# Optimization experiments

Measured on AMD Instinct MI355X. Metric: run time of the kernel, lower is better.

Reference implementation:

```python
import jax, jax.numpy as jnp
import numpy as np
from jax import lax

B, T, N, D = 64, 128, 64, 64
Q, EMB, PLM = 5, 8, 768
ALPHA = 0.5  # rarity_alpha

def _mlp(x, W1, b1, W2, b2):
    return jax.nn.relu(x @ W1 + b1) @ W2 + b2

def setup_inputs() -> dict:
    key = jax.random.key(0)
    ks = jax.random.split(key, 16)
    def xav(k, shape):
        fan_in = shape[-2] if len(shape) > 1 else shape[0]
        return jax.random.normal(k, shape, jnp.float32) / np.sqrt(fan_in)
    obs_emb = jax.random.normal(ks[0], (B, T, N, D), jnp.float32)
    observed_mask = (jax.random.uniform(ks[1], (B, T, N)) < 0.5).astype(jnp.float32)
    lengths = jax.random.randint(ks[2], (B, 1), T // 2, T + 1).astype(jnp.int32)
    lengths = lengths.at[0, 0].set(T)  # ensure max(lengths) == T like torch loop bound
    avg_interval = jax.random.uniform(ks[3], (B, T, N), jnp.float32) * 10.0
    return {
        "obs_emb": obs_emb, "observed_mask": observed_mask,
        "lengths": lengths, "avg_interval": avg_interval,
        "var_plm_rep": jax.random.normal(ks[4], (N, PLM), jnp.float32),
        "rarity_W": jax.random.normal(ks[5], (N, N), jnp.float32),
        "Wf1": xav(ks[6], (PLM, 2 * D)), "bf1": jnp.zeros((2 * D,), jnp.float32),
        "Wf2": xav(ks[7], (2 * D, Q)), "bf2": jnp.zeros((Q,), jnp.float32),
        "Wg1": xav(ks[8], (PLM, 2 * D)), "bg1": jnp.zeros((2 * D,), jnp.float32),
        "Wg2": xav(ks[9], (2 * D, EMB)), "bg2": jnp.zeros((EMB,), jnp.float32),
        "Wu": xav(ks[10], (Q, 2 * D + 1, D)), "bu": xav(ks[11], (Q, D)),
        "Wr": xav(ks[12], (Q, 2 * D + 1, D)), "br": xav(ks[13], (Q, D)),
        "Wc": xav(ks[14], (Q, 2 * D + 1, D)), "bc": xav(ks[15], (Q, D)),
    }

def reference(obs_emb, observed_mask, lengths, avg_interval, var_plm_rep, rarity_W,
              Wf1, bf1, Wf2, bf2, Wg1, bg1, Wg2, bg2, Wu, bu, Wr, br, Wc, bc):
    Bb, Tt, Nn, Dd = obs_emb.shape
    m_all = observed_mask.astype(obs_emb.dtype)                 # [B,T,N]
    # plm reps are repeated across batch in torch -> batch-identical, keep [N,*]
    qv = _mlp(var_plm_rep, Wf1, bf1, Wf2, bf2)                  # [N,Q]
    ne = _mlp(var_plm_rep, Wg1, bg1, Wg2, bg2)                  # [N,EMB]
    ne = ne / jnp.linalg.norm(ne, axis=-1, keepdims=True)
    adj = jax.nn.softmax(ne @ ne.T, axis=-1)                    # [N,N]
    # time-invariant per-node hypernetwork weights (MLP_Param einsums hoisted)
    Wr_n = jnp.einsum('nq,qio->nio', qv, Wr); br_n = qv @ br    # [N,2D+1,D],[N,D]
    Wu_n = jnp.einsum('nq,qio->nio', qv, Wu); bu_n = qv @ bu
    Wc_n = jnp.einsum('nq,qio->nio', qv, Wc); bc_n = qv @ bc
    I = jnp.eye(Nn, dtype=obs_emb.dtype)
    var_total = m_all.sum(axis=1)                               # [B,N]
    lens = lengths[:, 0]

    def step(carry, inp):
        h, out = carry
        x_t, m_t, ai_t, t = inp                                 # [B,N,D],[B,N],[B,N],[]
        rs = ALPHA * jnp.tanh(ai_t / (var_total + 1.0))         # rarity score [B,N]
        x = jnp.concatenate([x_t, rs[..., None]], axis=-1)      # [B,N,D+1]
        combined = jnp.concatenate([x, h], axis=-1)             # [B,N,2D+1]
        R = -rarity_W[None] * jnp.abs(rs[:, :, None] - rs[:, None, :])
        am = m_t[:, :, None] * m_t[:, None, :]                  # masked adjacency support
        A = adj[None] * (1.0 + R) * am * (1.0 - I) + I          # [B,N,N]
        msg = jnp.einsum('bij,bjf->bif', A, combined)           # dense message passing
        r = jax.nn.sigmoid(jnp.einsum('bnf,nfo->bno', msg, Wr_n) + br_n)
        u = jax.nn.sigmoid(jnp.einsum('bnf,nfo->bno', msg, Wu_n) + bu_n)
        upd = m_t[..., None] > 0                                # observed-node scatter mask
        h_r = jnp.where(upd, r * h, h)
        comb2 = jnp.concatenate([x, h_r], axis=-1)              # NOTE: no adj matmul here (as in torch)
        cand = jnp.tanh(jnp.einsum('bnf,nfo->bno', comb2, Wc_n) + bc_n)
        h_new = jnp.where(upd, (1.0 - u) * h_r + u * cand, h)
        out_new = jnp.where((t == lens - 1)[:, None, None], h_new, out)
        return (h_new, out_new), None

    h0 = jnp.zeros((Bb, Nn, Dd), obs_emb.dtype)
    xs = (obs_emb.swapaxes(0, 1), m_all.swapaxes(0, 1),
          avg_interval.swapaxes(0, 1), jnp.arange(Tt))
    (_, out), _ = lax.scan(step, (h0, jnp.zeros_like(h0)), xs)
    return out
```

## Files before the change

### kernel.cpp

```cpp
#include <hip/hip_runtime.h>
#include <cstddef>
#include <cstdint>

#define B_ 64
#define T_ 128
#define N_ 64
#define D_ 64
#define Q_ 5
#define E_ 8
#define P_ 768
#define H_ 128

typedef _Float16 f16;
typedef _Float16 f16x2 __attribute__((ext_vector_type(2)));
typedef _Float16 f16x4 __attribute__((ext_vector_type(4)));
typedef _Float16 f16x8 __attribute__((ext_vector_type(8)));
typedef float f32x4 __attribute__((ext_vector_type(4)));

__device__ __forceinline__ float fast_sig(float x) {
  return 1.f / (1.f + __expf(-x));
}
__device__ __forceinline__ float fast_tanh(float x) {
  return 1.f - 2.f / (1.f + __expf(2.f * x));
}
__device__ __forceinline__ f16x8 splat8(f16 c) {
  return f16x8{c, c, c, c, c, c, c, c};
}

__global__ void k_mlps(const float* __restrict__ vpr,
                       const float* __restrict__ Wf1, const float* __restrict__ bf1,
                       const float* __restrict__ Wf2, const float* __restrict__ bf2,
                       const float* __restrict__ Wg1, const float* __restrict__ bg1,
                       const float* __restrict__ Wg2, const float* __restrict__ bg2,
                       float* __restrict__ qv, float* __restrict__ neb) {
  int n = blockIdx.x;
  int tid = threadIdx.x;
  __shared__ float v[P_];
  __shared__ float hf[H_];
  __shared__ float hg[H_];
  __shared__ float tmp[E_];

  for (int i = tid; i < P_; i += 256) v[i] = vpr[n * P_ + i];
  __syncthreads();

  if (tid < H_) {
    int j = tid;
    float a = bf1[j];
#pragma unroll 8
    for (int i = 0; i < P_; ++i) a += v[i] * Wf1[i * H_ + j];
    hf[j] = fmaxf(a, 0.f);
  } else {
    int j = tid - H_;
    float a = bg1[j];
#pragma unroll 8
    for (int i = 0; i < P_; ++i) a += v[i] * Wg1[i * H_ + j];
    hg[j] = fmaxf(a, 0.f);
  }
  __syncthreads();
  if (tid < Q_) {
    float a = bf2[tid];
    for (int j = 0; j < H_; ++j) a += hf[j] * Wf2[j * Q_ + tid];
    qv[n * Q_ + tid] = a;
  } else if (tid >= 8 && tid < 8 + E_) {
    int e = tid - 8;
    float a = bg2[e];
    for (int j = 0; j < H_; ++j) a += hg[j] * Wg2[j * E_ + e];
    tmp[e] = a;
  }
  __syncthreads();
  if (tid == 0) {
    float s = 0.f;
    for (int e = 0; e < E_; ++e) s += tmp[e] * tmp[e];
    float r = 1.f / sqrtf(s);
    for (int e = 0; e < E_; ++e) neb[n * E_ + e] = tmp[e] * r;
  }
}

__global__ void k_meta(const float* __restrict__ neb, const float* __restrict__ qv,
                       const float* __restrict__ br, const float* __restrict__ bu,
                       const float* __restrict__ bc,
                       const float* __restrict__ Wr, const float* __restrict__ Wu,
                       const float* __restrict__ Wc, const float* __restrict__ rarw,
                       f16x2* __restrict__ adjP, float* __restrict__ brn,
                       float* __restrict__ bun, float* __restrict__ bcn,
                       float* __restrict__ WrsR, float* __restrict__ WrsU,
                       float* __restrict__ WrsC) {
  int n = blockIdx.x;
  int j = threadIdx.x;
  float s = 0.f;
#pragma unroll
  for (int e = 0; e < E_; ++e) s += neb[n * E_ + e] * neb[j * E_ + e];
  float m = s;
  for (int off = 32; off; off >>= 1) m = fmaxf(m, __shfl_xor(m, off));
  float ex = __expf(s - m);
  float sum = ex;
  for (int off = 32; off; off >>= 1) sum += __shfl_xor(sum, off);
  float av = ex / sum;
  adjP[n * N_ + j] = f16x2{(f16)av, (f16)(av * rarw[n * N_ + j])};

  float pr = 0.f, pu = 0.f, pc = 0.f;
  float wr = 0.f, wu = 0.f, wc = 0.f;
#pragma unroll
  for (int q = 0; q < Q_; ++q) {
    float qq = qv[n * Q_ + q];
    pr += qq * br[q * D_ + j];
    pu += qq * bu[q * D_ + j];
    pc += qq * bc[q * D_ + j];
    wr += qq * Wr[((size_t)q * 129 + 64) * D_ + j];
    wu += qq * Wu[((size_t)q * 129 + 64) * D_ + j];
    wc += qq * Wc[((size_t)q * 129 + 64) * D_ + j];
  }
  brn[n * D_ + j] = pr;
  bun[n * D_ + j] = pu;
  bcn[n * D_ + j] = pc;
  WrsR[n * D_ + j] = wr;
  WrsU[n * D_ + j] = wu;
  WrsC[n * D_ + j] = wc;
}

__global__ void k_pack(const float* __restrict__ Wr, const float* __restrict__ Wu,
                       const float* __restrict__ Wc, f16* __restrict__ Wpk) {
  int bid = blockIdx.x;
  int nt = bid & 3;
  int kt = (bid >> 2) & 3;
  int q = (bid >> 4) % 5;
  int g = bid / 80;
  const float* W = (g == 0) ? Wr : ((g == 1) ? Wu : Wc);
  int l = threadIdx.x;
  int co = 16 * nt + (l & 15);
  f16* dst = Wpk + (size_t)bid * 512 + l * 8;
#pragma unroll
  for (int e = 0; e < 8; ++e) {
    int k = 32 * kt + 8 * (l >> 4) + e;
    int f = k + (k >= 64);
    dst[e] = (f16)W[((size_t)q * 129 + f) * D_ + co];
  }
}

__global__ void k_vt(const float* __restrict__ mask, float* __restrict__ vt) {
  int b = blockIdx.x;
  int n = threadIdx.x;
  float s = 0.f;
  for (int t = 0; t < T_; ++t) s += mask[(b * T_ + t) * N_ + n];
  vt[b * N_ + n] = s;
}

__global__ __launch_bounds__(256, 1) __attribute__((amdgpu_waves_per_eu(1, 1)))
void k_seq(const float* __restrict__ obs, const float* __restrict__ mask,
           const int* __restrict__ lengths, const float* __restrict__ ai,
           const f16x2* __restrict__ adjP,
           const float* __restrict__ brn, const float* __restrict__ bun,
           const float* __restrict__ bcn, const float* __restrict__ WrsR,
           const float* __restrict__ WrsU, const float* __restrict__ WrsC,
           const float* __restrict__ qv, const float* __restrict__ vt,
           const f16* __restrict__ Wpk, float* __restrict__ out) {
  __shared__ __align__(16) f16 combT[128 * 72];
  __shared__ __align__(16) f16 xA[64 * 72];
  __shared__ __align__(16) f16 actA[64 * 168];
  __shared__ __align__(16) f16 AP[64 * 88];
  __shared__ __align__(16) f16 qvS[64 * 8];
  __shared__ __align__(16) float rsS[N_];
  __shared__ __align__(16) float mS[N_];
  __shared__ __align__(16) float mrS[N_];

  const int tid = threadIdx.x;
  const int b = blockIdx.x;
  const int lane = tid & 63;
  const int wv = tid >> 6;
  const int lm = lane & 15;
  const int lq = lane >> 4;
  const int oc = 16 * wv + lm;

  const int pn = tid >> 2;
  const int pj = 16 * (tid & 3);

  f16x8 wW[3][4][5];
#pragma unroll
  for (int g = 0; g < 3; ++g)
#pragma unroll
    for (int kt = 0; kt < 4; ++kt)
#pragma unroll
      for (int q = 0; q < 5; ++q)
        wW[g][kt][q] = *(const f16x8*)(Wpk +
            ((size_t)(((g * 5 + q) * 4 + kt) * 4 + wv) * 64 + lane) * 8);

  f16x2 bR[8], bU[8], bC[8], wRs[8], wUs[8], wCs[8];
#pragma unroll
  for (int mt = 0; mt < 4; ++mt)
#pragma unroll
    for (int ii = 0; ii < 2; ++ii) {
      int n0 = 16 * mt + 4 * lq + 2 * ii;
      bR[2 * mt + ii]  = f16x2{(f16)brn[n0 * D_ + oc],  (f16)brn[(n0 + 1) * D_ + oc]};
      bU[2 * mt + ii]  = f16x2{(f16)bun[n0 * D_ + oc],  (f16)bun[(n0 + 1) * D_ + oc]};
      bC[2 * mt + ii]  = f16x2{(f16)bcn[n0 * D_ + oc],  (f16)bcn[(n0 + 1) * D_ + oc]};
      wRs[2 * mt + ii] = f16x2{(f16)WrsR[n0 * D_ + oc], (f16)WrsR[(n0 + 1) * D_ + oc]};
      wUs[2 * mt + ii] = f16x2{(f16)WrsU[n0 * D_ + oc], (f16)WrsU[(n0 + 1) * D_ + oc]};
      wCs[2 * mt + ii] = f16x2{(f16)WrsC[n0 * D_ + oc], (f16)WrsC[(n0 + 1) * D_ + oc]};
    }

  f16x2 adjR[16];
#pragma unroll
  for (int k = 0; k < 16; ++k) adjR[k] = adjP[pn * N_ + pj + k];

#pragma unroll
  for (int u2 = 0; u2 < 2; ++u2) {
    int idx = 2 * tid + u2;
    int n = idx >> 3, q = idx & 7;
    qvS[idx] = (q < Q_) ? (f16)qv[n * Q_ + q] : (f16)0.f;
  }
  for (int i = tid; i < 64 * 72; i += 256) combT[64 * 72 + i] = (f16)0.f;

  f32x4 h[4];
#pragma unroll
  for (int mt = 0; mt < 4; ++mt) h[mt] = f32x4{0.f, 0.f, 0.f, 0.f};

  const float* xb = obs + (size_t)b * T_ * (N_ * D_) + pn * D_ + pj;
  float4 xq0 = *(const float4*)(xb);
  float4 xq1 = *(const float4*)(xb + 4);
  float4 xq2 = *(const float4*)(xb + 8);
  float4 xq3 = *(const float4*)(xb + 12);
  float mCur = 0.f, aCur = 0.f, vtR = 0.f;
  if (tid < N_) {
    vtR = vt[b * N_ + tid];
    mCur = mask[(size_t)b * T_ * N_ + tid];
    aCur = ai[(size_t)b * T_ * N_ + tid];
  }
  const int lenm1 = lengths[b] - 1;
  __syncthreads();

  f16x8 qh[4];
#pragma unroll
  for (int mt = 0; mt < 4; ++mt) qh[mt] = *(const f16x8*)(qvS + (lm + 16 * mt) * 8);

  for (int t = 0; t < T_; ++t) {
    if (tid < N_) {
      mS[tid] = mCur;
      rsS[tid] = 0.5f * fast_tanh(aCur / (vtR + 1.f));
    }
    {
      f16x8 v0 = {(f16)xq0.x, (f16)xq0.y, (f16)xq0.z, (f16)xq0.w,
                  (f16)xq1.x, (f16)xq1.y, (f16)xq1.z, (f16)xq1.w};
      f16x8 v1 = {(f16)xq2.x, (f16)xq2.y, (f16)xq2.z, (f16)xq2.w,
                  (f16)xq3.x, (f16)xq3.y, (f16)xq3.z, (f16)xq3.w};
      *(f16x8*)(xA + pn * 72 + pj) = v0;
      *(f16x8*)(xA + pn * 72 + pj + 8) = v1;
    }
    __syncthreads();

    {
      float ri = rsS[pn], mi = mS[pn];
      f16x8 av0, av1;
#pragma unroll
      for (int k = 0; k < 16; ++k) {
        float a = ((float)adjR[k][0] -
                   (float)adjR[k][1] * fabsf(ri - rsS[pj + k])) * mi * mS[pj + k];
        if (pn == pj + k) a = 1.f;
        if (k < 8) av0[k] = (f16)a;
        else av1[k - 8] = (f16)a;
      }
      *(f16x8*)(AP + pn * 88 + pj) = av0;
      *(f16x8*)(AP + pn * 88 + pj + 8) = av1;

      int n0 = 16 * wv;
      f16x8 t0, t1;
#pragma unroll
      for (int k = 0; k < 8; ++k) t0[k] = xA[(n0 + k) * 72 + lane];
#pragma unroll
      for (int k = 0; k < 8; ++k) t1[k] = xA[(n0 + 8 + k) * 72 + lane];
      *(f16x8*)(combT + lane * 72 + n0) = t0;
      *(f16x8*)(combT + lane * 72 + n0 + 8) = t1;
    }
    __syncthreads();

    {
#pragma unroll
      for (int s = 0; s < 2; ++s) {
        int ft = 2 * wv + s;
#pragma unroll
        for (int mt = 0; mt < 4; ++mt) {
          f32x4 acc = {0.f, 0.f, 0.f, 0.f};
#pragma unroll
          for (int kt = 0; kt < 2; ++kt) {
            f16x8 aF = *(const f16x8*)(AP + (lm + 16 * mt) * 88 + 8 * lq + 32 * kt);
            f16x8 bF = *(const f16x8*)(combT + (lm + 16 * ft) * 72 + 8 * lq + 32 * kt);
            acc = __builtin_amdgcn_mfma_f32_16x16x32_f16(aF, bF, acc, 0, 0, 0);
          }
          int row = 16 * mt + 4 * lq;
          int col = 16 * ft + lm;
          actA[(row + 0) * 168 + col] = (f16)acc[0];
          actA[(row + 1) * 168 + col] = (f16)acc[1];
          actA[(row + 2) * 168 + col] = (f16)acc[2];
          actA[(row + 3) * 168 + col] = (f16)acc[3];
        }
      }
      f16x8 a0 = *(const f16x8*)(AP + pn * 88 + pj);
      f16x8 a1 = *(const f16x8*)(AP + pn * 88 + pj + 8);
      float s = 0.f;
#pragma unroll
      for (int k = 0; k < 8; ++k)
        s += (float)a0[k] * rsS[pj + k] + (float)a1[k] * rsS[pj + 8 + k];
      s += __shfl_xor(s, 1);
      s += __shfl_xor(s, 2);
      if ((tid & 3) == 0) mrS[pn] = s;
    }
    __syncthreads();

    f32x4 racc[4], uacc[4];
#pragma unroll
    for (int mt = 0; mt < 4; ++mt) {
      racc[mt] = f32x4{0.f, 0.f, 0.f, 0.f};
      uacc[mt] = f32x4{0.f, 0.f, 0.f, 0.f};
    }
#pragma unroll
    for (int kt = 0; kt < 4; ++kt) {
      f16x8 aF[4];
#pragma unroll
      for (int mt = 0; mt < 4; ++mt)
        aF[mt] = *(const f16x8*)(actA + (lm + 16 * mt) * 168 + 8 * lq + 32 * kt);
#pragma unroll
      for (int q = 0; q < 5; ++q) {
#pragma unroll
        for (int mt = 0; mt < 4; ++mt) {
          f16x8 as = aF[mt] * splat8(qh[mt][q]);
          racc[mt] = __builtin_amdgcn_mfma_f32_16x16x32_f16(as, wW[0][kt][q], racc[mt], 0, 0, 0);
          uacc[mt] = __builtin_amdgcn_mfma_f32_16x16x32_f16(as, wW[1][kt][q], uacc[mt], 0, 0, 0);
        }
      }
    }

    f16x2 upk[8], hrpk[8];
    {
#pragma unroll
      for (int mt = 0; mt < 4; ++mt) {
        float4 mr4 = *(const float4*)&mrS[16 * mt + 4 * lq];
        float4 m4 = *(const float4*)&mS[16 * mt + 4 * lq];
#pragma unroll
        for (int i = 0; i < 4; ++i) {
          int row = 16 * mt + 4 * lq + i;
          int ii = 2 * mt + (i >> 1);
          float pr = racc[mt][i] + (float)bR[ii][i & 1] + mr4[i] * (float)wRs[ii][i & 1];
          float pu = uacc[mt][i] + (float)bU[ii][i & 1] + mr4[i] * (float)wUs[ii][i & 1];
          float r = fast_sig(pr);
          float u = fast_sig(pu);
          float hr = (m4[i] > 0.f) ? r * h[mt][i] : h[mt][i];
          upk[ii][i & 1] = (f16)u;
          hrpk[ii][i & 1] = (f16)hr;
          AP[row * 88 + oc] = (f16)hr;
        }
      }
      if (t + 1 < T_) {
        const float* xn = xb + (size_t)(t + 1) * (N_ * D_);
        xq0 = *(const float4*)(xn);
        xq1 = *(const float4*)(xn + 4);
        xq2 = *(const float4*)(xn + 8);
        xq3 = *(const float4*)(xn + 12);
        if (tid < N_) {
          mCur = mask[((size_t)b * T_ + t + 1) * N_ + tid];
          aCur = ai[((size_t)b * T_ + t + 1) * N_ + tid];
        }
      }
    }
    __syncthreads();

    f32x4 cacc[4];
#pragma unroll
    for (int mt = 0; mt < 4; ++mt) cacc[mt] = f32x4{0.f, 0.f, 0.f, 0.f};
#pragma unroll
    for (int kt = 0; kt < 4; ++kt) {
      f16x8 aF[4];
#pragma unroll
      for (int mt = 0; mt < 4; ++mt) {
        if (kt < 2)
          aF[mt] = *(const f16x8*)(xA + (lm + 16 * mt) * 72 + 8 * lq + 32 * kt);
        else
          aF[mt] = *(const f16x8*)(AP + (lm + 16 * mt) * 88 + 8 * lq + 32 * (kt - 2));
      }
#pragma unroll
      for (int q = 0; q < 5; ++q) {
#pragma unroll
        for (int mt = 0; mt < 4; ++mt) {
          f16x8 as = aF[mt] * splat8(qh[mt][q]);
          cacc[mt] = __builtin_amdgcn_mfma_f32_16x16x32_f16(as, wW[2][kt][q], cacc[mt], 0, 0, 0);
        }
      }
    }

    {
#pragma unroll
      for (int mt = 0; mt < 4; ++mt) {
        float4 rs4 = *(const float4*)&rsS[16 * mt + 4 * lq];
        float4 m4 = *(const float4*)&mS[16 * mt + 4 * lq];
        f16x4 hq;
#pragma unroll
        for (int i = 0; i < 4; ++i) {
          int ii = 2 * mt + (i >> 1);
          float pc = cacc[mt][i] + (float)bC[ii][i & 1] + rs4[i] * (float)wCs[ii][i & 1];
          float cand = fast_tanh(pc);
          float u = (float)upk[ii][i & 1];
          float hr = (float)hrpk[ii][i & 1];
          float hn = (m4[i] > 0.f) ? (1.f - u) * hr + u * cand : h[mt][i];
          h[mt][i] = hn;
          hq[i] = (f16)hn;
        }
        *(f16x4*)(combT + (64 + oc) * 72 + 16 * mt + 4 * lq) = hq;
        if (t == lenm1) {
#pragma unroll
          for (int i = 0; i < 4; ++i)
            out[((size_t)b * N_ + 16 * mt + 4 * lq + i) * D_ + oc] = h[mt][i];
        }
      }
    }
    __syncthreads();
  }
}

extern "C" void kernel_launch(void* const* d_in, const int* in_sizes, int n_in,
                              void* d_out, int out_size, void* d_ws, size_t ws_size,
                              hipStream_t stream) {
  const float* obs  = (const float*)d_in[0];
  const float* mask = (const float*)d_in[1];
  const int*   lens = (const int*)d_in[2];
  const float* ai   = (const float*)d_in[3];
  const float* vpr  = (const float*)d_in[4];
  const float* rarw = (const float*)d_in[5];
  const float* Wf1 = (const float*)d_in[6],  *bf1 = (const float*)d_in[7];
  const float* Wf2 = (const float*)d_in[8],  *bf2 = (const float*)d_in[9];
  const float* Wg1 = (const float*)d_in[10], *bg1 = (const float*)d_in[11];
  const float* Wg2 = (const float*)d_in[12], *bg2 = (const float*)d_in[13];
  const float* Wu = (const float*)d_in[14], *bu = (const float*)d_in[15];
  const float* Wr = (const float*)d_in[16], *br = (const float*)d_in[17];
  const float* Wc = (const float*)d_in[18], *bc = (const float*)d_in[19];

  char* p = (char*)d_ws;
  auto carve = [&](size_t bytes) {
    char* r = p;
    p += (bytes + 255) & ~(size_t)255;
    return r;
  };
  float* qv   = (float*)carve(N_ * Q_ * 4);
  float* neb  = (float*)carve(N_ * E_ * 4);
  f16x2* adjP = (f16x2*)carve(N_ * N_ * 4);
  float* brn  = (float*)carve(N_ * D_ * 4);
  float* bun  = (float*)carve(N_ * D_ * 4);
  float* bcn  = (float*)carve(N_ * D_ * 4);
  float* WrsR = (float*)carve(N_ * D_ * 4);
  float* WrsU = (float*)carve(N_ * D_ * 4);
  float* WrsC = (float*)carve(N_ * D_ * 4);
  float* vt   = (float*)carve(B_ * N_ * 4);
  f16* Wpk    = (f16*)carve((size_t)3 * 5 * 4 * 4 * 64 * 8 * 2);

  k_mlps<<<N_, 256, 0, stream>>>(vpr, Wf1, bf1, Wf2, bf2, Wg1, bg1, Wg2, bg2, qv, neb);
  k_meta<<<N_, 64, 0, stream>>>(neb, qv, br, bu, bc, Wr, Wu, Wc, rarw,
                                adjP, brn, bun, bcn, WrsR, WrsU, WrsC);
  k_pack<<<240, 64, 0, stream>>>(Wr, Wu, Wc, Wpk);
  k_vt<<<B_, 64, 0, stream>>>(mask, vt);
  k_seq<<<B_, 256, 0, stream>>>(obs, mask, lens, ai, adjP,
                                brn, bun, bcn, WrsR, WrsU, WrsC,
                                qv, vt, Wpk, (float*)d_out);
}
```

Measured before the change: 2.146 ms.

## Split recurrent GRU matmuls across 8 waves with split-K LDS reduction

Doubles the recurrent kernel's block from 256 to 512 threads. The two wave groups each take half of the K dimension of the gate and candidate MFMA chains, and the upper group's partial accumulators are summed into the lower group's through a shared-memory buffer. Per-node bias and rarity weights move from registers to padded shared-memory tables to free registers, and the adjacency and transpose prep is spread over more threads. This is meant to shorten the serial per-timestep MFMA latency. In exchange it adds a reduction buffer, extra barriers per step, and leaves half the waves idle during the elementwise gate phases.

```diff
diff --git a/kernel.cpp b/kernel.cpp
--- a/kernel.cpp
+++ b/kernel.cpp
@@ -145,7 +145,9 @@
   vt[b * N_ + n] = s;
 }
 
-__global__ __launch_bounds__(256, 1) __attribute__((amdgpu_waves_per_eu(1, 1)))
+#define BSTR 68
+
+__global__ __launch_bounds__(512, 2)
 void k_seq(const float* __restrict__ obs, const float* __restrict__ mask,
            const int* __restrict__ lengths, const float* __restrict__ ai,
            const f16x2* __restrict__ adjP,
@@ -162,53 +164,52 @@
   __shared__ __align__(16) float rsS[N_];
   __shared__ __align__(16) float mS[N_];
   __shared__ __align__(16) float mrS[N_];
+  __shared__ __align__(16) float red[32 * 256];
+  __shared__ __align__(16) f16 bRl[64 * BSTR], bUl[64 * BSTR], bCl[64 * BSTR];
+  __shared__ __align__(16) f16 wRl[64 * BSTR], wUl[64 * BSTR], wCl[64 * BSTR];
 
   const int tid = threadIdx.x;
   const int b = blockIdx.x;
   const int lane = tid & 63;
   const int wv = tid >> 6;
+  const int lo = wv & 3;
+  const int hi = wv >> 2;
   const int lm = lane & 15;
   const int lq = lane >> 4;
-  const int oc = 16 * wv + lm;
-
-  const int pn = tid >> 2;
-  const int pj = 16 * (tid & 3);
-
-  f16x8 wW[3][4][5];
+  const int oc = 16 * lo + lm;
+
+  const int pn = tid >> 3;
+  const int pj = (tid & 7) * 8;
+
+  f16x8 wW[3][2][5];
 #pragma unroll
   for (int g = 0; g < 3; ++g)
 #pragma unroll
-    for (int kt = 0; kt < 4; ++kt)
+    for (int ktl = 0; ktl < 2; ++ktl)
 #pragma unroll
       for (int q = 0; q < 5; ++q)
-        wW[g][kt][q] = *(const f16x8*)(Wpk +
-            ((size_t)(((g * 5 + q) * 4 + kt) * 4 + wv) * 64 + lane) * 8);
-
-  f16x2 bR[8], bU[8], bC[8], wRs[8], wUs[8], wCs[8];
-#pragma unroll
-  for (int mt = 0; mt < 4; ++mt)
-#pragma unroll
-    for (int ii = 0; ii < 2; ++ii) {
-      int n0 = 16 * mt + 4 * lq + 2 * ii;
-      bR[2 * mt + ii]  = f16x2{(f16)brn[n0 * D_ + oc],  (f16)brn[(n0 + 1) * D_ + oc]};
-      bU[2 * mt + ii]  = f16x2{(f16)bun[n0 * D_ + oc],  (f16)bun[(n0 + 1) * D_ + oc]};
-      bC[2 * mt + ii]  = f16x2{(f16)bcn[n0 * D_ + oc],  (f16)bcn[(n0 + 1) * D_ + oc]};
-      wRs[2 * mt + ii] = f16x2{(f16)WrsR[n0 * D_ + oc], (f16)WrsR[(n0 + 1) * D_ + oc]};
-      wUs[2 * mt + ii] = f16x2{(f16)WrsU[n0 * D_ + oc], (f16)WrsU[(n0 + 1) * D_ + oc]};
-      wCs[2 * mt + ii] = f16x2{(f16)WrsC[n0 * D_ + oc], (f16)WrsC[(n0 + 1) * D_ + oc]};
-    }
-
-  f16x2 adjR[16];
-#pragma unroll
-  for (int k = 0; k < 16; ++k) adjR[k] = adjP[pn * N_ + pj + k];
-
-#pragma unroll
-  for (int u2 = 0; u2 < 2; ++u2) {
-    int idx = 2 * tid + u2;
-    int n = idx >> 3, q = idx & 7;
-    qvS[idx] = (q < Q_) ? (f16)qv[n * Q_ + q] : (f16)0.f;
-  }
-  for (int i = tid; i < 64 * 72; i += 256) combT[64 * 72 + i] = (f16)0.f;
+        wW[g][ktl][q] = *(const f16x8*)(Wpk +
+            ((size_t)(((g * 5 + q) * 4 + (2 * hi + ktl)) * 4 + lo) * 64 + lane) * 8);
+
+  f16x2 adjR[8];
+#pragma unroll
+  for (int k = 0; k < 8; ++k) adjR[k] = adjP[pn * N_ + pj + k];
+
+  for (int i = tid; i < 64 * 64; i += 512) {
+    int o = i >> 6, n = i & 63;
+    bRl[o * BSTR + n] = (f16)brn[n * D_ + o];
+    bUl[o * BSTR + n] = (f16)bun[n * D_ + o];
+    bCl[o * BSTR + n] = (f16)bcn[n * D_ + o];
+    wRl[o * BSTR + n] = (f16)WrsR[n * D_ + o];
+    wUl[o * BSTR + n] = (f16)WrsU[n * D_ + o];
+    wCl[o * BSTR + n] = (f16)WrsC[n * D_ + o];
+  }
+
+  {
+    int n = tid >> 3, q = tid & 7;
+    qvS[tid] = (q < Q_) ? (f16)qv[n * Q_ + q] : (f16)0.f;
+  }
+  for (int i = tid; i < 64 * 72; i += 512) combT[64 * 72 + i] = (f16)0.f;
 
   f32x4 h[4];
 #pragma unroll
@@ -217,8 +218,6 @@
   const float* xb = obs + (size_t)b * T_ * (N_ * D_) + pn * D_ + pj;
   float4 xq0 = *(const float4*)(xb);
   float4 xq1 = *(const float4*)(xb + 4);
-  float4 xq2 = *(const float4*)(xb + 8);
-  float4 xq3 = *(const float4*)(xb + 12);
   float mCur = 0.f, aCur = 0.f, vtR = 0.f;
   if (tid < N_) {
     vtR = vt[b * N_ + tid];
@@ -240,68 +239,55 @@
     {
       f16x8 v0 = {(f16)xq0.x, (f16)xq0.y, (f16)xq0.z, (f16)xq0.w,
                   (f16)xq1.x, (f16)xq1.y, (f16)xq1.z, (f16)xq1.w};
-      f16x8 v1 = {(f16)xq2.x, (f16)xq2.y, (f16)xq2.z, (f16)xq2.w,
-                  (f16)xq3.x, (f16)xq3.y, (f16)xq3.z, (f16)xq3.w};
       *(f16x8*)(xA + pn * 72 + pj) = v0;
-      *(f16x8*)(xA + pn * 72 + pj + 8) = v1;
     }
     __syncthreads();
 
     {
       float ri = rsS[pn], mi = mS[pn];
-      f16x8 av0, av1;
-#pragma unroll
-      for (int k = 0; k < 16; ++k) {
+      f16x8 av;
+#pragma unroll
+      for (int k = 0; k < 8; ++k) {
         float a = ((float)adjR[k][0] -
                    (float)adjR[k][1] * fabsf(ri - rsS[pj + k])) * mi * mS[pj + k];
         if (pn == pj + k) a = 1.f;
-        if (k < 8) av0[k] = (f16)a;
-        else av1[k - 8] = (f16)a;
-      }
-      *(f16x8*)(AP + pn * 88 + pj) = av0;
-      *(f16x8*)(AP + pn * 88 + pj + 8) = av1;
-
-      int n0 = 16 * wv;
-      f16x8 t0, t1;
+        av[k] = (f16)a;
+      }
+      *(f16x8*)(AP + pn * 88 + pj) = av;
+
+      int n0 = 8 * wv;
+      f16x8 t0;
 #pragma unroll
       for (int k = 0; k < 8; ++k) t0[k] = xA[(n0 + k) * 72 + lane];
-#pragma unroll
-      for (int k = 0; k < 8; ++k) t1[k] = xA[(n0 + 8 + k) * 72 + lane];
       *(f16x8*)(combT + lane * 72 + n0) = t0;
-      *(f16x8*)(combT + lane * 72 + n0 + 8) = t1;
     }
     __syncthreads();
 
     {
 #pragma unroll
-      for (int s = 0; s < 2; ++s) {
-        int ft = 2 * wv + s;
-#pragma unroll
-        for (int mt = 0; mt < 4; ++mt) {
-          f32x4 acc = {0.f, 0.f, 0.f, 0.f};
-#pragma unroll
-          for (int kt = 0; kt < 2; ++kt) {
-            f16x8 aF = *(const f16x8*)(AP + (lm + 16 * mt) * 88 + 8 * lq + 32 * kt);
-            f16x8 bF = *(const f16x8*)(combT + (lm + 16 * ft) * 72 + 8 * lq + 32 * kt);
-            acc = __builtin_amdgcn_mfma_f32_16x16x32_f16(aF, bF, acc, 0, 0, 0);
-          }
-          int row = 16 * mt + 4 * lq;
-          int col = 16 * ft + lm;
-          actA[(row + 0) * 168 + col] = (f16)acc[0];
-          actA[(row + 1) * 168 + col] = (f16)acc[1];
-          actA[(row + 2) * 168 + col] = (f16)acc[2];
-          actA[(row + 3) * 168 + col] = (f16)acc[3];
-        }
+      for (int mt = 0; mt < 4; ++mt) {
+        f32x4 acc = {0.f, 0.f, 0.f, 0.f};
+#pragma unroll
+        for (int kt = 0; kt < 2; ++kt) {
+          f16x8 aF = *(const f16x8*)(AP + (lm + 16 * mt) * 88 + 8 * lq + 32 * kt);
+          f16x8 bF = *(const f16x8*)(combT + (lm + 16 * wv) * 72 + 8 * lq + 32 * kt);
+          acc = __builtin_amdgcn_mfma_f32_16x16x32_f16(aF, bF, acc, 0, 0, 0);
+        }
+        int row = 16 * mt + 4 * lq;
+        int col = 16 * wv + lm;
+        actA[(row + 0) * 168 + col] = (f16)acc[0];
+        actA[(row + 1) * 168 + col] = (f16)acc[1];
+        actA[(row + 2) * 168 + col] = (f16)acc[2];
+        actA[(row + 3) * 168 + col] = (f16)acc[3];
       }
       f16x8 a0 = *(const f16x8*)(AP + pn * 88 + pj);
-      f16x8 a1 = *(const f16x8*)(AP + pn * 88 + pj + 8);
       float s = 0.f;
 #pragma unroll
-      for (int k = 0; k < 8; ++k)
-        s += (float)a0[k] * rsS[pj + k] + (float)a1[k] * rsS[pj + 8 + k];
+      for (int k = 0; k < 8; ++k) s += (float)a0[k] * rsS[pj + k];
       s += __shfl_xor(s, 1);
       s += __shfl_xor(s, 2);
-      if ((tid & 3) == 0) mrS[pn] = s;
+      s += __shfl_xor(s, 4);
+      if ((tid & 7) == 0) mrS[pn] = s;
     }
     __syncthreads();
 
@@ -312,52 +298,68 @@
       uacc[mt] = f32x4{0.f, 0.f, 0.f, 0.f};
     }
 #pragma unroll
-    for (int kt = 0; kt < 4; ++kt) {
+    for (int ktl = 0; ktl < 2; ++ktl) {
       f16x8 aF[4];
 #pragma unroll
       for (int mt = 0; mt < 4; ++mt)
-        aF[mt] = *(const f16x8*)(actA + (lm + 16 * mt) * 168 + 8 * lq + 32 * kt);
+        aF[mt] = *(const f16x8*)(actA + (lm + 16 * mt) * 168 + 8 * lq +
+                                 32 * (2 * hi + ktl));
 #pragma unroll
       for (int q = 0; q < 5; ++q) {
 #pragma unroll
         for (int mt = 0; mt < 4; ++mt) {
           f16x8 as = aF[mt] * splat8(qh[mt][q]);
-          racc[mt] = __builtin_amdgcn_mfma_f32_16x16x32_f16(as, wW[0][kt][q], racc[mt], 0, 0, 0);
-          uacc[mt] = __builtin_amdgcn_mfma_f32_16x16x32_f16(as, wW[1][kt][q], uacc[mt], 0, 0, 0);
-        }
-      }
-    }
+          racc[mt] = __builtin_amdgcn_mfma_f32_16x16x32_f16(as, wW[0][ktl][q], racc[mt], 0, 0, 0);
+          uacc[mt] = __builtin_amdgcn_mfma_f32_16x16x32_f16(as, wW[1][ktl][q], uacc[mt], 0, 0, 0);
+        }
+      }
+    }
+    if (hi) {
+      int u = tid & 255;
+#pragma unroll
+      for (int mt = 0; mt < 4; ++mt)
+#pragma unroll
+        for (int i = 0; i < 4; ++i) {
+          red[(mt * 4 + i) * 256 + u] = racc[mt][i];
+          red[(16 + mt * 4 + i) * 256 + u] = uacc[mt][i];
+        }
+    }
+    __syncthreads();
 
     f16x2 upk[8], hrpk[8];
-    {
+    if (hi == 0) {
 #pragma unroll
       for (int mt = 0; mt < 4; ++mt) {
-        float4 mr4 = *(const float4*)&mrS[16 * mt + 4 * lq];
-        float4 m4 = *(const float4*)&mS[16 * mt + 4 * lq];
+        int nb = 16 * mt + 4 * lq;
+        float4 mr4 = *(const float4*)&mrS[nb];
+        float4 m4 = *(const float4*)&mS[nb];
+        f16x4 bRv = *(const f16x4*)(bRl + oc * BSTR + nb);
+        f16x4 wRv = *(const f16x4*)(wRl + oc * BSTR + nb);
+        f16x4 bUv = *(const f16x4*)(bUl + oc * BSTR + nb);
+        f16x4 wUv = *(const f16x4*)(wUl + oc * BSTR + nb);
 #pragma unroll
         for (int i = 0; i < 4; ++i) {
-          int row = 16 * mt + 4 * lq + i;
           int ii = 2 * mt + (i >> 1);
-          float pr = racc[mt][i] + (float)bR[ii][i & 1] + mr4[i] * (float)wRs[ii][i & 1];
-          float pu = uacc[mt][i] + (float)bU[ii][i & 1] + mr4[i] * (float)wUs[ii][i & 1];
+          float pr = racc[mt][i] + red[(mt * 4 + i) * 256 + tid] +
+                     (float)bRv[i] + mr4[i] * (float)wRv[i];
+          float pu = uacc[mt][i] + red[(16 + mt * 4 + i) * 256 + tid] +
+                     (float)bUv[i] + mr4[i] * (float)wUv[i];
           float r = fast_sig(pr);
           float u = fast_sig(pu);
           float hr = (m4[i] > 0.f) ? r * h[mt][i] : h[mt][i];
           upk[ii][i & 1] = (f16)u;
           hrpk[ii][i & 1] = (f16)hr;
-          AP[row * 88 + oc] = (f16)hr;
-        }
-      }
-      if (t + 1 < T_) {
-        const float* xn = xb + (size_t)(t + 1) * (N_ * D_);
-        xq0 = *(const float4*)(xn);
-        xq1 = *(const float4*)(xn + 4);
-        xq2 = *(const float4*)(xn + 8);
-        xq3 = *(const float4*)(xn + 12);
-        if (tid < N_) {
-          mCur = mask[((size_t)b * T_ + t + 1) * N_ + tid];
-          aCur = ai[((size_t)b * T_ + t + 1) * N_ + tid];
-        }
+          AP[(nb + i) * 88 + oc] = (f16)hr;
+        }
+      }
+    }
+    if (t + 1 < T_) {
+      const float* xn = xb + (size_t)(t + 1) * (N_ * D_);
+      xq0 = *(const float4*)(xn);
+      xq1 = *(const float4*)(xn + 4);
+      if (tid < N_) {
+        mCur = mask[((size_t)b * T_ + t + 1) * N_ + tid];
+        aCur = ai[((size_t)b * T_ + t + 1) * N_ + tid];
       }
     }
     __syncthreads();
@@ -366,35 +368,48 @@
 #pragma unroll
     for (int mt = 0; mt < 4; ++mt) cacc[mt] = f32x4{0.f, 0.f, 0.f, 0.f};
 #pragma unroll
-    for (int kt = 0; kt < 4; ++kt) {
+    for (int ktl = 0; ktl < 2; ++ktl) {
       f16x8 aF[4];
 #pragma unroll
       for (int mt = 0; mt < 4; ++mt) {
-        if (kt < 2)
-          aF[mt] = *(const f16x8*)(xA + (lm + 16 * mt) * 72 + 8 * lq + 32 * kt);
+        if (hi == 0)
+          aF[mt] = *(const f16x8*)(xA + (lm + 16 * mt) * 72 + 8 * lq + 32 * ktl);
         else
-          aF[mt] = *(const f16x8*)(AP + (lm + 16 * mt) * 88 + 8 * lq + 32 * (kt - 2));
+          aF[mt] = *(const f16x8*)(AP + (lm + 16 * mt) * 88 + 8 * lq + 32 * ktl);
       }
 #pragma unroll
       for (int q = 0; q < 5; ++q) {
 #pragma unroll
         for (int mt = 0; mt < 4; ++mt) {
           f16x8 as = aF[mt] * splat8(qh[mt][q]);
-          cacc[mt] = __builtin_amdgcn_mfma_f32_16x16x32_f16(as, wW[2][kt][q], cacc[mt], 0, 0, 0);
-        }
-      }
-    }
-
-    {
+          cacc[mt] = __builtin_amdgcn_mfma_f32_16x16x32_f16(as, wW[2][ktl][q], cacc[mt], 0, 0, 0);
+        }
+      }
+    }
+    if (hi) {
+      int u = tid & 255;
+#pragma unroll
+      for (int mt = 0; mt < 4; ++mt)
+#pragma unroll
+        for (int i = 0; i < 4; ++i)
+          red[(mt * 4 + i) * 256 + u] = cacc[mt][i];
+    }
+    __syncthreads();
+
+    if (hi == 0) {
 #pragma unroll
       for (int mt = 0; mt < 4; ++mt) {
-        float4 rs4 = *(const float4*)&rsS[16 * mt + 4 * lq];
-        float4 m4 = *(const float4*)&mS[16 * mt + 4 * lq];
+        int nb = 16 * mt + 4 * lq;
+        float4 rs4 = *(const float4*)&rsS[nb];
+        float4 m4 = *(const float4*)&mS[nb];
+        f16x4 bCv = *(const f16x4*)(bCl + oc * BSTR + nb);
+        f16x4 wCv = *(const f16x4*)(wCl + oc * BSTR + nb);
         f16x4 hq;
 #pragma unroll
         for (int i = 0; i < 4; ++i) {
           int ii = 2 * mt + (i >> 1);
-          float pc = cacc[mt][i] + (float)bC[ii][i & 1] + rs4[i] * (float)wCs[ii][i & 1];
+          float pc = cacc[mt][i] + red[(mt * 4 + i) * 256 + tid] +
+                     (float)bCv[i] + rs4[i] * (float)wCv[i];
           float cand = fast_tanh(pc);
           float u = (float)upk[ii][i & 1];
           float hr = (float)hrpk[ii][i & 1];
@@ -402,11 +417,11 @@
           h[mt][i] = hn;
           hq[i] = (f16)hn;
         }
-        *(f16x4*)(combT + (64 + oc) * 72 + 16 * mt + 4 * lq) = hq;
+        *(f16x4*)(combT + (64 + oc) * 72 + nb) = hq;
         if (t == lenm1) {
 #pragma unroll
           for (int i = 0; i < 4; ++i)
-            out[((size_t)b * N_ + 16 * mt + 4 * lq + i) * D_ + oc] = h[mt][i];
+            out[((size_t)b * N_ + nb + i) * D_ + oc] = h[mt][i];
         }
       }
     }
@@ -454,7 +469,7 @@
                                 adjP, brn, bun, bcn, WrsR, WrsU, WrsC);
   k_pack<<<240, 64, 0, stream>>>(Wr, Wu, Wc, Wpk);
   k_vt<<<B_, 64, 0, stream>>>(mask, vt);
-  k_seq<<<B_, 256, 0, stream>>>(obs, mask, lens, ai, adjP,
+  k_seq<<<B_, 512, 0, stream>>>(obs, mask, lens, ai, adjP,
                                 brn, bun, bcn, WrsR, WrsU, WrsC,
                                 qv, vt, Wpk, (float*)d_out);
 }
```

After: 4.890 ms. 128% more time.

## Double-buffer per-step inputs and split candidate GEMM to cut barriers per timestep

Applied to the files above, without the earlier changes.

Double-buffers xA, AP, mS and rsS so the next timestep's inputs, adjacency and transposed x are built inside the current step, overlapping with MFMA work. The candidate GEMM is split into an x half that runs before a barrier and an h_r half that runs after it. This reduces the per-step barrier count from five to three and moves global-load latency off the critical path. It costs extra LDS and adds a write-after-read hazard on combT that relies on barrier ordering.

```diff
diff --git a/kernel.cpp b/kernel.cpp
--- a/kernel.cpp
+++ b/kernel.cpp
@@ -155,12 +155,12 @@
            const float* __restrict__ qv, const float* __restrict__ vt,
            const f16* __restrict__ Wpk, float* __restrict__ out) {
   __shared__ __align__(16) f16 combT[128 * 72];
-  __shared__ __align__(16) f16 xA[64 * 72];
+  __shared__ __align__(16) f16 xA[2][64 * 72];
   __shared__ __align__(16) f16 actA[64 * 168];
-  __shared__ __align__(16) f16 AP[64 * 88];
+  __shared__ __align__(16) f16 AP[2][64 * 88];
   __shared__ __align__(16) f16 qvS[64 * 8];
-  __shared__ __align__(16) float rsS[N_];
-  __shared__ __align__(16) float mS[N_];
+  __shared__ __align__(16) float rsS[2][N_];
+  __shared__ __align__(16) float mS[2][N_];
   __shared__ __align__(16) float mrS[N_];
 
   const int tid = threadIdx.x;
@@ -215,15 +215,25 @@
   for (int mt = 0; mt < 4; ++mt) h[mt] = f32x4{0.f, 0.f, 0.f, 0.f};
 
   const float* xb = obs + (size_t)b * T_ * (N_ * D_) + pn * D_ + pj;
-  float4 xq0 = *(const float4*)(xb);
-  float4 xq1 = *(const float4*)(xb + 4);
-  float4 xq2 = *(const float4*)(xb + 8);
-  float4 xq3 = *(const float4*)(xb + 12);
-  float mCur = 0.f, aCur = 0.f, vtR = 0.f;
+  {
+    float4 x0 = *(const float4*)(xb);
+    float4 x1 = *(const float4*)(xb + 4);
+    float4 x2 = *(const float4*)(xb + 8);
+    float4 x3 = *(const float4*)(xb + 12);
+    f16x8 v0 = {(f16)x0.x, (f16)x0.y, (f16)x0.z, (f16)x0.w,
+                (f16)x1.x, (f16)x1.y, (f16)x1.z, (f16)x1.w};
+    f16x8 v1 = {(f16)x2.x, (f16)x2.y, (f16)x2.z, (f16)x2.w,
+                (f16)x3.x, (f16)x3.y, (f16)x3.z, (f16)x3.w};
+    *(f16x8*)(xA[0] + pn * 72 + pj) = v0;
+    *(f16x8*)(xA[0] + pn * 72 + pj + 8) = v1;
+  }
+  float vtR = 0.f;
   if (tid < N_) {
     vtR = vt[b * N_ + tid];
-    mCur = mask[(size_t)b * T_ * N_ + tid];
-    aCur = ai[(size_t)b * T_ * N_ + tid];
+    float mC = mask[(size_t)b * T_ * N_ + tid];
+    float aC = ai[(size_t)b * T_ * N_ + tid];
+    mS[0][tid] = mC;
+    rsS[0][tid] = 0.5f * fast_tanh(aC / (vtR + 1.f));
   }
   const int lenm1 = lengths[b] - 1;
   __syncthreads();
@@ -232,45 +242,33 @@
 #pragma unroll
   for (int mt = 0; mt < 4; ++mt) qh[mt] = *(const f16x8*)(qvS + (lm + 16 * mt) * 8);
 
+  {
+    int n0 = 16 * wv;
+    f16x8 t0, t1;
+#pragma unroll
+    for (int k = 0; k < 8; ++k) t0[k] = xA[0][(n0 + k) * 72 + lane];
+#pragma unroll
+    for (int k = 0; k < 8; ++k) t1[k] = xA[0][(n0 + 8 + k) * 72 + lane];
+    *(f16x8*)(combT + lane * 72 + n0) = t0;
+    *(f16x8*)(combT + lane * 72 + n0 + 8) = t1;
+
+    float ri = rsS[0][pn], mi = mS[0][pn];
+    f16x8 av0, av1;
+#pragma unroll
+    for (int k = 0; k < 16; ++k) {
+      float a = ((float)adjR[k][0] -
+                 (float)adjR[k][1] * fabsf(ri - rsS[0][pj + k])) * mi * mS[0][pj + k];
+      if (pn == pj + k) a = 1.f;
+      if (k < 8) av0[k] = (f16)a;
+      else av1[k - 8] = (f16)a;
+    }
+    *(f16x8*)(AP[0] + pn * 88 + pj) = av0;
+    *(f16x8*)(AP[0] + pn * 88 + pj + 8) = av1;
+  }
+  __syncthreads();
+
   for (int t = 0; t < T_; ++t) {
-    if (tid < N_) {
-      mS[tid] = mCur;
-      rsS[tid] = 0.5f * fast_tanh(aCur / (vtR + 1.f));
-    }
-    {
-      f16x8 v0 = {(f16)xq0.x, (f16)xq0.y, (f16)xq0.z, (f16)xq0.w,
-                  (f16)xq1.x, (f16)xq1.y, (f16)xq1.z, (f16)xq1.w};
-      f16x8 v1 = {(f16)xq2.x, (f16)xq2.y, (f16)xq2.z, (f16)xq2.w,
-                  (f16)xq3.x, (f16)xq3.y, (f16)xq3.z, (f16)xq3.w};
-      *(f16x8*)(xA + pn * 72 + pj) = v0;
-      *(f16x8*)(xA + pn * 72 + pj + 8) = v1;
-    }
-    __syncthreads();
-
-    {
-      float ri = rsS[pn], mi = mS[pn];
-      f16x8 av0, av1;
-#pragma unroll
-      for (int k = 0; k < 16; ++k) {
-        float a = ((float)adjR[k][0] -
-                   (float)adjR[k][1] * fabsf(ri - rsS[pj + k])) * mi * mS[pj + k];
-        if (pn == pj + k) a = 1.f;
-        if (k < 8) av0[k] = (f16)a;
-        else av1[k - 8] = (f16)a;
-      }
-      *(f16x8*)(AP + pn * 88 + pj) = av0;
-      *(f16x8*)(AP + pn * 88 + pj + 8) = av1;
-
-      int n0 = 16 * wv;
-      f16x8 t0, t1;
-#pragma unroll
-      for (int k = 0; k < 8; ++k) t0[k] = xA[(n0 + k) * 72 + lane];
-#pragma unroll
-      for (int k = 0; k < 8; ++k) t1[k] = xA[(n0 + 8 + k) * 72 + lane];
-      *(f16x8*)(combT + lane * 72 + n0) = t0;
-      *(f16x8*)(combT + lane * 72 + n0 + 8) = t1;
-    }
-    __syncthreads();
+    const int cur = t & 1, nxt = cur ^ 1;
 
     {
 #pragma unroll
@@ -281,7 +279,7 @@
           f32x4 acc = {0.f, 0.f, 0.f, 0.f};
 #pragma unroll
           for (int kt = 0; kt < 2; ++kt) {
-            f16x8 aF = *(const f16x8*)(AP + (lm + 16 * mt) * 88 + 8 * lq + 32 * kt);
+            f16x8 aF = *(const f16x8*)(AP[cur] + (lm + 16 * mt) * 88 + 8 * lq + 32 * kt);
             f16x8 bF = *(const f16x8*)(combT + (lm + 16 * ft) * 72 + 8 * lq + 32 * kt);
             acc = __builtin_amdgcn_mfma_f32_16x16x32_f16(aF, bF, acc, 0, 0, 0);
           }
@@ -293,18 +291,31 @@
           actA[(row + 3) * 168 + col] = (f16)acc[3];
         }
       }
-      f16x8 a0 = *(const f16x8*)(AP + pn * 88 + pj);
-      f16x8 a1 = *(const f16x8*)(AP + pn * 88 + pj + 8);
+      f16x8 a0 = *(const f16x8*)(AP[cur] + pn * 88 + pj);
+      f16x8 a1 = *(const f16x8*)(AP[cur] + pn * 88 + pj + 8);
       float s = 0.f;
 #pragma unroll
       for (int k = 0; k < 8; ++k)
-        s += (float)a0[k] * rsS[pj + k] + (float)a1[k] * rsS[pj + 8 + k];
+        s += (float)a0[k] * rsS[cur][pj + k] + (float)a1[k] * rsS[cur][pj + 8 + k];
       s += __shfl_xor(s, 1);
       s += __shfl_xor(s, 2);
       if ((tid & 3) == 0) mrS[pn] = s;
     }
     __syncthreads();
 
+    float4 nx0, nx1, nx2, nx3;
+    float mN = 0.f, aN = 0.f;
+    if (t + 1 < T_) {
+      const float* xn = xb + (size_t)(t + 1) * (N_ * D_);
+      nx0 = *(const float4*)(xn);
+      nx1 = *(const float4*)(xn + 4);
+      nx2 = *(const float4*)(xn + 8);
+      nx3 = *(const float4*)(xn + 12);
+      if (tid < N_) {
+        mN = mask[((size_t)b * T_ + t + 1) * N_ + tid];
+        aN = ai[((size_t)b * T_ + t + 1) * N_ + tid];
+      }
+    }
     f32x4 racc[4], uacc[4];
 #pragma unroll
     for (int mt = 0; mt < 4; ++mt) {
@@ -327,13 +338,12 @@
         }
       }
     }
-
     f16x2 upk[8], hrpk[8];
     {
 #pragma unroll
       for (int mt = 0; mt < 4; ++mt) {
         float4 mr4 = *(const float4*)&mrS[16 * mt + 4 * lq];
-        float4 m4 = *(const float4*)&mS[16 * mt + 4 * lq];
+        float4 m4 = *(const float4*)&mS[cur][16 * mt + 4 * lq];
 #pragma unroll
         for (int i = 0; i < 4; ++i) {
           int row = 16 * mt + 4 * lq + i;
@@ -345,36 +355,19 @@
           float hr = (m4[i] > 0.f) ? r * h[mt][i] : h[mt][i];
           upk[ii][i & 1] = (f16)u;
           hrpk[ii][i & 1] = (f16)hr;
-          AP[row * 88 + oc] = (f16)hr;
-        }
-      }
-      if (t + 1 < T_) {
-        const float* xn = xb + (size_t)(t + 1) * (N_ * D_);
-        xq0 = *(const float4*)(xn);
-        xq1 = *(const float4*)(xn + 4);
-        xq2 = *(const float4*)(xn + 8);
-        xq3 = *(const float4*)(xn + 12);
-        if (tid < N_) {
-          mCur = mask[((size_t)b * T_ + t + 1) * N_ + tid];
-          aCur = ai[((size_t)b * T_ + t + 1) * N_ + tid];
-        }
-      }
-    }
-    __syncthreads();
-
+          AP[cur][row * 88 + oc] = (f16)hr;
+        }
+      }
+    }
     f32x4 cacc[4];
 #pragma unroll
     for (int mt = 0; mt < 4; ++mt) cacc[mt] = f32x4{0.f, 0.f, 0.f, 0.f};
 #pragma unroll
-    for (int kt = 0; kt < 4; ++kt) {
+    for (int kt = 0; kt < 2; ++kt) {
       f16x8 aF[4];
 #pragma unroll
-      for (int mt = 0; mt < 4; ++mt) {
-        if (kt < 2)
-          aF[mt] = *(const f16x8*)(xA + (lm + 16 * mt) * 72 + 8 * lq + 32 * kt);
-        else
-          aF[mt] = *(const f16x8*)(AP + (lm + 16 * mt) * 88 + 8 * lq + 32 * (kt - 2));
-      }
+      for (int mt = 0; mt < 4; ++mt)
+        aF[mt] = *(const f16x8*)(xA[cur] + (lm + 16 * mt) * 72 + 8 * lq + 32 * kt);
 #pragma unroll
       for (int q = 0; q < 5; ++q) {
 #pragma unroll
@@ -384,12 +377,40 @@
         }
       }
     }
-
+    if (t + 1 < T_) {
+      f16x8 v0 = {(f16)nx0.x, (f16)nx0.y, (f16)nx0.z, (f16)nx0.w,
+                  (f16)nx1.x, (f16)nx1.y, (f16)nx1.z, (f16)nx1.w};
+      f16x8 v1 = {(f16)nx2.x, (f16)nx2.y, (f16)nx2.z, (f16)nx2.w,
+                  (f16)nx3.x, (f16)nx3.y, (f16)nx3.z, (f16)nx3.w};
+      *(f16x8*)(xA[nxt] + pn * 72 + pj) = v0;
+      *(f16x8*)(xA[nxt] + pn * 72 + pj + 8) = v1;
+      if (tid < N_) {
+        mS[nxt][tid] = mN;
+        rsS[nxt][tid] = 0.5f * fast_tanh(aN / (vtR + 1.f));
+      }
+    }
+    __syncthreads();
+
+#pragma unroll
+    for (int kt = 0; kt < 2; ++kt) {
+      f16x8 aF[4];
+#pragma unroll
+      for (int mt = 0; mt < 4; ++mt)
+        aF[mt] = *(const f16x8*)(AP[cur] + (lm + 16 * mt) * 88 + 8 * lq + 32 * kt);
+#pragma unroll
+      for (int q = 0; q < 5; ++q) {
+#pragma unroll
+        for (int mt = 0; mt < 4; ++mt) {
+          f16x8 as = aF[mt] * splat8(qh[mt][q]);
+          cacc[mt] = __builtin_amdgcn_mfma_f32_16x16x32_f16(as, wW[2][kt + 2][q], cacc[mt], 0, 0, 0);
+        }
+      }
+    }
     {
 #pragma unroll
       for (int mt = 0; mt < 4; ++mt) {
-        float4 rs4 = *(const float4*)&rsS[16 * mt + 4 * lq];
-        float4 m4 = *(const float4*)&mS[16 * mt + 4 * lq];
+        float4 rs4 = *(const float4*)&rsS[cur][16 * mt + 4 * lq];
+        float4 m4 = *(const float4*)&mS[cur][16 * mt + 4 * lq];
         f16x4 hq;
 #pragma unroll
         for (int i = 0; i < 4; ++i) {
@@ -409,6 +430,29 @@
             out[((size_t)b * N_ + 16 * mt + 4 * lq + i) * D_ + oc] = h[mt][i];
         }
       }
+    }
+    if (t + 1 < T_) {
+      float ri = rsS[nxt][pn], mi = mS[nxt][pn];
+      f16x8 av0, av1;
+#pragma unroll
+      for (int k = 0; k < 16; ++k) {
+        float a = ((float)adjR[k][0] -
+                   (float)adjR[k][1] * fabsf(ri - rsS[nxt][pj + k])) * mi * mS[nxt][pj + k];
+        if (pn == pj + k) a = 1.f;
+        if (k < 8) av0[k] = (f16)a;
+        else av1[k - 8] = (f16)a;
+      }
+      *(f16x8*)(AP[nxt] + pn * 88 + pj) = av0;
+      *(f16x8*)(AP[nxt] + pn * 88 + pj + 8) = av1;
+
+      int n0 = 16 * wv;
+      f16x8 t0, t1;
+#pragma unroll
+      for (int k = 0; k < 8; ++k) t0[k] = xA[nxt][(n0 + k) * 72 + lane];
+#pragma unroll
+      for (int k = 0; k < 8; ++k) t1[k] = xA[nxt][(n0 + 8 + k) * 72 + lane];
+      *(f16x8*)(combT + lane * 72 + n0) = t0;
+      *(f16x8*)(combT + lane * 72 + n0 + 8) = t1;
     }
     __syncthreads();
   }
```

New measurement: 2.138 ms. About the same (-0.4%).
